# Optimization experiments

Hardware: AMD Instinct MI355X
Metric: run time of the kernel (lower is better)

Reference implementation:

```python
import jax, jax.numpy as jnp
import numpy as np

B, T, HE, H = 32, 2048, 512, 512


def setup_inputs() -> dict:
    key = jax.random.key(0)
    ks = jax.random.split(key, 10)
    s_e = 1.0 / np.sqrt(HE)
    s_h = 1.0 / np.sqrt(H)
    return {
        "x": jax.random.normal(ks[0], (B, T, HE), dtype=jnp.float32),
        "wu_i": jax.random.normal(ks[1], (HE, H), dtype=jnp.float32) * s_e,
        "wu_h": jax.random.normal(ks[2], (H, H), dtype=jnp.float32) * s_h,
        "bu": jax.random.normal(ks[3], (H,), dtype=jnp.float32) * s_h,
        "wr_i": jax.random.normal(ks[4], (HE, H), dtype=jnp.float32) * s_e,
        "wr_h": jax.random.normal(ks[5], (H, H), dtype=jnp.float32) * s_h,
        "br": jax.random.normal(ks[6], (H,), dtype=jnp.float32) * s_h,
        "wc_i": jax.random.normal(ks[7], (HE, H), dtype=jnp.float32) * s_e,
        "wc_h": jax.random.normal(ks[8], (H, H), dtype=jnp.float32) * s_h,
        "bc": jax.random.normal(ks[9], (H,), dtype=jnp.float32) * s_h,
    }


def reference(x, wu_i, wu_h, bu, wr_i, wr_h, br, wc_i, wc_h, bc):
    # Precompute input projections for all timesteps (one big GEMM each).
    u_in_x = jnp.einsum("bte,eh->bth", x, wu_i) + bu  # (B,T,H)
    r_in_x = jnp.einsum("bte,eh->bth", x, wr_i) + br
    c_in_x = jnp.einsum("bte,eh->bth", x, wc_i) + bc

    h0 = jnp.zeros((x.shape[0], wu_h.shape[0]), dtype=x.dtype)

    def step(h_prev, inputs):
        u_x, r_x, c_x = inputs
        u = jax.nn.sigmoid(u_x + h_prev @ wu_h)
        r = jax.nn.sigmoid(r_x + h_prev @ wr_h)
        # Faithful to source: r * (h_prev @ wc_h) (reset applied after matmul)
        c = jnp.tanh(c_x + r * (h_prev @ wc_h))
        h = (1.0 - u) * h_prev + u * c
        return h, h

    # scan over time: move T to leading axis
    xs = (
        jnp.swapaxes(u_in_x, 0, 1),
        jnp.swapaxes(r_in_x, 0, 1),
        jnp.swapaxes(c_in_x, 0, 1),
    )
    _, ys = jax.lax.scan(step, h0, xs)  # ys: (T,B,H)
    return jnp.swapaxes(ys, 0, 1)  # (B,T,H)
```

## Files before the change

### kernel.cpp

```cpp
#include <hip/hip_runtime.h>
#include <hip/hip_bf16.h>
#include <hip/hip_fp16.h>
#include <stdint.h>

#define BB 32
#define TT 2048
#define HH 512
#define MM (BB*TT)

typedef __attribute__((ext_vector_type(8))) short bf16x8;
typedef __attribute__((ext_vector_type(4))) float f32x4;
typedef __attribute__((ext_vector_type(2))) float f32x2;
typedef __attribute__((ext_vector_type(4))) unsigned short us4;
typedef __attribute__((ext_vector_type(8))) unsigned short us8;
typedef unsigned long long u64;

__device__ __forceinline__ unsigned short f2bf(float f) {
  __hip_bfloat16 h = __float2bfloat16(f);
  return *reinterpret_cast<unsigned short*>(&h);
}
__device__ __forceinline__ float bf2f(unsigned short u) {
  return __uint_as_float(((unsigned int)u) << 16);
}

__device__ __forceinline__ void wg_barrier_lgkm() {
  asm volatile("s_waitcnt lgkmcnt(0)\n\ts_barrier" ::: "memory");
}

__device__ __forceinline__ float fast_sigmoid(float x) {
  float e = __expf(-x);
  return __builtin_amdgcn_rcpf(1.f + e);
}
__device__ __forceinline__ float fast_tanh(float x) {
  float xc = fminf(fmaxf(x, -15.f), 15.f);
  float e2 = __expf(2.f * xc);
  return (e2 - 1.f) * __builtin_amdgcn_rcpf(e2 + 1.f);
}

__global__ void wconv_kernel(const float* __restrict__ wu, const float* __restrict__ wr,
                             const float* __restrict__ wc,
                             unsigned short* __restrict__ wuT, unsigned short* __restrict__ wrT,
                             unsigned short* __restrict__ wcTh, unsigned short* __restrict__ wcTl) {
  int idx = blockIdx.x * 256 + threadIdx.x;
  int n = idx >> 9, k = idx & 511;
  int src = k * HH + n;
  wuT[idx] = f2bf(wu[src]);
  wrT[idx] = f2bf(wr[src]);
  float v = wc[src];
  unsigned short hi = f2bf(v);
  wcTh[idx] = hi;
  wcTl[idx] = f2bf(v - bf2f(hi));
}

template<int MODE>
__global__ __launch_bounds__(256) void proj_gemm(
    const float* __restrict__ X,
    const unsigned short* __restrict__ B0T,
    const unsigned short* __restrict__ B1T,
    const float* __restrict__ bias0,
    const float* __restrict__ bias1,
    void* __restrict__ outp) {
  __shared__ __attribute__((aligned(16))) unsigned short Ah[128][72];
  __shared__ __attribute__((aligned(16))) unsigned short Al[128][72];
  __shared__ __attribute__((aligned(16))) unsigned short Bs0[64][72];
  __shared__ __attribute__((aligned(16))) unsigned short Bs1[64][72];
  const int tid = threadIdx.x;
  const int w = tid >> 6, l = tid & 63;
  const int lr = l & 15, lk = l >> 4;
  const int rowBase = blockIdx.x * 128;
  const int colBase = blockIdx.y * 64;

  f32x4 acc0[2][4], acc1[2][4];
  const f32x4 zero = {0.f, 0.f, 0.f, 0.f};
  #pragma unroll
  for (int m = 0; m < 2; ++m)
    #pragma unroll
    for (int n = 0; n < 4; ++n) { acc0[m][n] = zero; acc1[m][n] = zero; }

  for (int kt = 0; kt < 8; ++kt) {
    #pragma unroll
    for (int i = 0; i < 8; ++i) {
      int idx = tid + 256 * i;
      int r = idx >> 4, c4 = idx & 15;
      float4 v = *reinterpret_cast<const float4*>(
          X + (size_t)(rowBase + r) * HH + kt * 64 + c4 * 4);
      us4 hv;
      hv.x = f2bf(v.x); hv.y = f2bf(v.y); hv.z = f2bf(v.z); hv.w = f2bf(v.w);
      *reinterpret_cast<us4*>(&Ah[r][c4 * 4]) = hv;
      if (MODE == 1) {
        us4 lv;
        lv.x = f2bf(v.x - bf2f(hv.x)); lv.y = f2bf(v.y - bf2f(hv.y));
        lv.z = f2bf(v.z - bf2f(hv.z)); lv.w = f2bf(v.w - bf2f(hv.w));
        *reinterpret_cast<us4*>(&Al[r][c4 * 4]) = lv;
      }
    }
    #pragma unroll
    for (int i = 0; i < 2; ++i) {
      int idx = tid + 256 * i;
      int n = idx >> 3, k8 = idx & 7;
      const size_t go = (size_t)(colBase + n) * HH + kt * 64 + k8 * 8;
      *reinterpret_cast<us8*>(&Bs0[n][k8 * 8]) = *reinterpret_cast<const us8*>(B0T + go);
      *reinterpret_cast<us8*>(&Bs1[n][k8 * 8]) = *reinterpret_cast<const us8*>(B1T + go);
    }
    __syncthreads();
    #pragma unroll
    for (int ks = 0; ks < 2; ++ks) {
      const int k0 = ks * 32 + lk * 8;
      bf16x8 a[2], b0[4], b1[4];
      #pragma unroll
      for (int m = 0; m < 2; ++m)
        a[m] = *reinterpret_cast<const bf16x8*>(&Ah[32 * w + 16 * m + lr][k0]);
      #pragma unroll
      for (int n = 0; n < 4; ++n) {
        b0[n] = *reinterpret_cast<const bf16x8*>(&Bs0[16 * n + lr][k0]);
        b1[n] = *reinterpret_cast<const bf16x8*>(&Bs1[16 * n + lr][k0]);
      }
      if (MODE == 1) {
        bf16x8 al[2];
        #pragma unroll
        for (int m = 0; m < 2; ++m)
          al[m] = *reinterpret_cast<const bf16x8*>(&Al[32 * w + 16 * m + lr][k0]);
        #pragma unroll
        for (int m = 0; m < 2; ++m)
          #pragma unroll
          for (int n = 0; n < 4; ++n) {
            acc0[m][n] = __builtin_amdgcn_mfma_f32_16x16x32_bf16(a[m],  b0[n], acc0[m][n], 0, 0, 0);
            acc0[m][n] = __builtin_amdgcn_mfma_f32_16x16x32_bf16(a[m],  b1[n], acc0[m][n], 0, 0, 0);
            acc0[m][n] = __builtin_amdgcn_mfma_f32_16x16x32_bf16(al[m], b0[n], acc0[m][n], 0, 0, 0);
          }
      } else {
        #pragma unroll
        for (int m = 0; m < 2; ++m)
          #pragma unroll
          for (int n = 0; n < 4; ++n) {
            acc0[m][n] = __builtin_amdgcn_mfma_f32_16x16x32_bf16(a[m], b0[n], acc0[m][n], 0, 0, 0);
            acc1[m][n] = __builtin_amdgcn_mfma_f32_16x16x32_bf16(a[m], b1[n], acc1[m][n], 0, 0, 0);
          }
      }
    }
    __syncthreads();
  }
  #pragma unroll
  for (int m = 0; m < 2; ++m) {
    #pragma unroll
    for (int n = 0; n < 4; ++n) {
      const int col = colBase + 16 * n + lr;
      const float bv0 = bias0[col];
      const float bv1 = (MODE == 0) ? bias1[col] : 0.f;
      #pragma unroll
      for (int q = 0; q < 4; ++q) {
        const int row = rowBase + 32 * w + 16 * m + lk * 4 + q;
        const size_t o = (size_t)row * HH + col;
        if (MODE == 0) {
          float v0 = acc0[m][n][q] + bv0;
          float v1 = acc1[m][n][q] + bv1;
          unsigned int pk = (unsigned int)__half_as_ushort(__float2half(v0)) |
                            ((unsigned int)__half_as_ushort(__float2half(v1)) << 16);
          reinterpret_cast<unsigned int*>(outp)[o] = pk;
        } else {
          reinterpret_cast<__half*>(outp)[o] = __float2half(acc0[m][n][q] + bv0);
        }
      }
    }
  }
}

__global__ __launch_bounds__(512, 2) void scan_kernel(
    const float* __restrict__ wu_h, const float* __restrict__ wr_h,
    const float* __restrict__ wc_h,
    float* __restrict__ out, const __half* __restrict__ cx,
    u64* __restrict__ hslow) {
  const int blk = blockIdx.x;
  const int b = (blk & 7) + ((blk >> 6) << 3);
  const int g = (blk >> 3) & 7;
  const int tid = threadIdx.x;
  const int w = tid >> 6, l = tid & 63;
  const int jg = g * 64 + l;
  const int jp = w * 64 + l;
  const size_t bo = (size_t)b * TT * HH;

  f32x2 wu2[32], wr2[32], wc2[32];
  #pragma unroll
  for (int i = 0; i < 32; ++i) {
    const size_t o0 = (size_t)(w * 64 + 2 * i) * HH + jg;
    wu2[i] = f32x2{wu_h[o0], wu_h[o0 + HH]};
    wr2[i] = f32x2{wr_h[o0], wr_h[o0 + HH]};
    wc2[i] = f32x2{wc_h[o0], wc_h[o0 + HH]};
  }

  __shared__ float parts[2][8][3][64];
  __shared__ unsigned int  stag_urx[64];
  __shared__ unsigned short stag_cx[64];

  unsigned int* outu = reinterpret_cast<unsigned int*>(out);
  const unsigned short* cxu = reinterpret_cast<const unsigned short*>(cx);

  unsigned int urx_p = 0;
  unsigned short cx_p = 0;
  if (w == 1) {
    urx_p = outu[bo + jg];
    cx_p  = cxu[bo + jg];
  }

  float hprev = 0.f;
  u64* const poll = hslow + (size_t)b * HH + jp;
  u64* const pub  = hslow + (size_t)b * HH + jg;
  const bool out_duty = (g == 1);

  for (int t = 0; t < TT; ++t) {
    float hval = 0.f;
    if (t > 0) {
      u64 v;
      for (;;) {
        v = __hip_atomic_load(poll + (size_t)(t & 1) * (BB * HH),
                              __ATOMIC_RELAXED, __HIP_MEMORY_SCOPE_AGENT);
        if (__all((int)((unsigned int)(v >> 32) >= (unsigned int)t))) break;
      }
      hval = __uint_as_float((unsigned int)v);
      if (out_duty)
        out[bo + (size_t)(t - 1) * HH + jp] = hval;
    }
    if (w == 1) {
      stag_urx[l] = urx_p;
      stag_cx[l]  = cx_p;
      if (t + 1 < TT) {
        urx_p = outu[bo + (size_t)(t + 1) * HH + jg];
        cx_p  = cxu[bo + (size_t)(t + 1) * HH + jg];
      }
    }
    f32x2 au2 = {0.f, 0.f}, ar2 = {0.f, 0.f}, ac2 = {0.f, 0.f};
    const unsigned int hbits = __float_as_uint(hval);
    #pragma unroll
    for (int i = 0; i < 32; ++i) {
      f32x2 hp;
      hp.x = __uint_as_float(__builtin_amdgcn_readlane(hbits, 2 * i));
      hp.y = __uint_as_float(__builtin_amdgcn_readlane(hbits, 2 * i + 1));
      au2 = __builtin_elementwise_fma(hp, wu2[i], au2);
      ar2 = __builtin_elementwise_fma(hp, wr2[i], ar2);
      ac2 = __builtin_elementwise_fma(hp, wc2[i], ac2);
    }
    const int pb = t & 1;
    parts[pb][w][0][l] = au2.x + au2.y;
    parts[pb][w][1][l] = ar2.x + ar2.y;
    parts[pb][w][2][l] = ac2.x + ac2.y;
    wg_barrier_lgkm();
    if (w == 0) {
      float su = 0.f, sr = 0.f, sc = 0.f;
      #pragma unroll
      for (int ww = 0; ww < 8; ++ww) {
        su += parts[pb][ww][0][l];
        sr += parts[pb][ww][1][l];
        sc += parts[pb][ww][2][l];
      }
      const unsigned int urx_c = stag_urx[l];
      const unsigned short cx_c = stag_cx[l];
      const float ux = __half2float(__ushort_as_half((unsigned short)(urx_c & 0xffffu)));
      const float rx = __half2float(__ushort_as_half((unsigned short)(urx_c >> 16)));
      const float cxf = __half2float(__ushort_as_half(cx_c));
      const float uu = fast_sigmoid(su + ux);
      const float rr = fast_sigmoid(sr + rx);
      const float ccv = fast_tanh(cxf + rr * sc);
      const float h = hprev + uu * (ccv - hprev);
      hprev = h;
      const u64 pv = ((u64)(unsigned int)(t + 1) << 32) | (u64)__float_as_uint(h);
      __hip_atomic_store(pub + (size_t)((t + 1) & 1) * (BB * HH), pv,
                         __ATOMIC_RELAXED, __HIP_MEMORY_SCOPE_AGENT);
    }
  }
  if (w == 0)
    out[bo + (size_t)(TT - 1) * HH + jg] = hprev;
}

extern "C" void kernel_launch(void* const* d_in, const int* in_sizes, int n_in,
                              void* d_out, int out_size, void* d_ws, size_t ws_size,
                              hipStream_t stream) {
  const float* x    = (const float*)d_in[0];
  const float* wu_i = (const float*)d_in[1];
  const float* wu_h = (const float*)d_in[2];
  const float* bu   = (const float*)d_in[3];
  const float* wr_i = (const float*)d_in[4];
  const float* wr_h = (const float*)d_in[5];
  const float* br   = (const float*)d_in[6];
  const float* wc_i = (const float*)d_in[7];
  const float* wc_h = (const float*)d_in[8];
  const float* bc   = (const float*)d_in[9];
  float* out = (float*)d_out;

  char* ws = (char*)d_ws;
  __half* cx = (__half*)ws;
  unsigned short* wuT  = (unsigned short*)(ws + (size_t)MM * HH * 2);
  unsigned short* wrT  = wuT + HH * HH;
  unsigned short* wcTh = wrT + HH * HH;
  unsigned short* wcTl = wcTh + HH * HH;
  u64* hslow = (u64*)(wcTl + HH * HH);

  hipMemsetAsync(hslow, 0, (size_t)2 * BB * HH * sizeof(u64), stream);
  wconv_kernel<<<1024, 256, 0, stream>>>(wu_i, wr_i, wc_i, wuT, wrT, wcTh, wcTl);
  proj_gemm<0><<<dim3(MM / 128, 8), 256, 0, stream>>>(x, wuT, wrT, bu, br, (void*)out);
  proj_gemm<1><<<dim3(MM / 128, 8), 256, 0, stream>>>(x, wcTh, wcTl, bc, bc, (void*)cx);

  void* args[] = { (void*)&wu_h, (void*)&wr_h, (void*)&wc_h, (void*)&out,
                   (void*)&cx, (void*)&hslow };
  hipLaunchCooperativeKernel((void*)scan_kernel, dim3(256), dim3(512), args, 0, stream);
}
```

Baseline: 3.714 ms.

## Distribute gate reduction across all waves and double-buffer staging

The cross-wave reduction and gate computation, previously done serially by wave 0 over 8 partial sums, is now spread across all 8 waves. Each wave owns 8 columns, and eight row-groups of 8 lanes each take one wave's partial and combine them with xor shuffles. The staging buffers become double-buffered by timestep parity, which makes the single-barrier schedule safe. The spin-poll keeps two loads in flight to cut the latency of seeing a new state. The goal is to shorten the serial critical path per timestep, at the cost of extra shuffles and padded shared memory.

```diff
diff --git a/kernel.cpp b/kernel.cpp
--- a/kernel.cpp
+++ b/kernel.cpp
@@ -35,6 +35,10 @@
   float xc = fminf(fmaxf(x, -15.f), 15.f);
   float e2 = __expf(2.f * xc);
   return (e2 - 1.f) * __builtin_amdgcn_rcpf(e2 + 1.f);
+}
+
+__device__ __forceinline__ u64 agent_ld(const u64* p) {
+  return __hip_atomic_load(p, __ATOMIC_RELAXED, __HIP_MEMORY_SCOPE_AGENT);
 }
 
 __global__ void wconv_kernel(const float* __restrict__ wu, const float* __restrict__ wr,
@@ -177,6 +181,9 @@
   const int w = tid >> 6, l = tid & 63;
   const int jg = g * 64 + l;
   const int jp = w * 64 + l;
+  const int cl = l & 7;
+  const int colw = 8 * w + cl;
+  const int pprime = l >> 3;
   const size_t bo = (size_t)b * TT * HH;
 
   f32x2 wu2[32], wr2[32], wc2[32];
@@ -188,9 +195,9 @@
     wc2[i] = f32x2{wc_h[o0], wc_h[o0 + HH]};
   }
 
-  __shared__ float parts[2][8][3][64];
-  __shared__ unsigned int  stag_urx[64];
-  __shared__ unsigned short stag_cx[64];
+  __shared__ float parts[2][8][3][72];
+  __shared__ unsigned int  stag_urx[2][64];
+  __shared__ unsigned short stag_cx[2][64];
 
   unsigned int* outu = reinterpret_cast<unsigned int*>(out);
   const unsigned short* cxu = reinterpret_cast<const unsigned short*>(cx);
@@ -204,25 +211,30 @@
 
   float hprev = 0.f;
   u64* const poll = hslow + (size_t)b * HH + jp;
-  u64* const pub  = hslow + (size_t)b * HH + jg;
+  u64* const pub  = hslow + (size_t)b * HH + 64 * g + colw;
   const bool out_duty = (g == 1);
 
   for (int t = 0; t < TT; ++t) {
+    const int pb = t & 1;
     float hval = 0.f;
     if (t > 0) {
+      const u64* pp = poll + (size_t)pb * (BB * HH);
+      u64 va = agent_ld(pp);
+      u64 vb = agent_ld(pp);
       u64 v;
       for (;;) {
-        v = __hip_atomic_load(poll + (size_t)(t & 1) * (BB * HH),
-                              __ATOMIC_RELAXED, __HIP_MEMORY_SCOPE_AGENT);
-        if (__all((int)((unsigned int)(v >> 32) >= (unsigned int)t))) break;
+        if (__all((int)((unsigned int)(va >> 32) >= (unsigned int)t))) { v = va; break; }
+        va = agent_ld(pp);
+        if (__all((int)((unsigned int)(vb >> 32) >= (unsigned int)t))) { v = vb; break; }
+        vb = agent_ld(pp);
       }
       hval = __uint_as_float((unsigned int)v);
       if (out_duty)
         out[bo + (size_t)(t - 1) * HH + jp] = hval;
     }
     if (w == 1) {
-      stag_urx[l] = urx_p;
-      stag_cx[l]  = cx_p;
+      stag_urx[pb][l] = urx_p;
+      stag_cx[pb][l]  = cx_p;
       if (t + 1 < TT) {
         urx_p = outu[bo + (size_t)(t + 1) * HH + jg];
         cx_p  = cxu[bo + (size_t)(t + 1) * HH + jg];
@@ -239,36 +251,36 @@
       ar2 = __builtin_elementwise_fma(hp, wr2[i], ar2);
       ac2 = __builtin_elementwise_fma(hp, wc2[i], ac2);
     }
-    const int pb = t & 1;
     parts[pb][w][0][l] = au2.x + au2.y;
     parts[pb][w][1][l] = ar2.x + ar2.y;
     parts[pb][w][2][l] = ac2.x + ac2.y;
     wg_barrier_lgkm();
-    if (w == 0) {
-      float su = 0.f, sr = 0.f, sc = 0.f;
-      #pragma unroll
-      for (int ww = 0; ww < 8; ++ww) {
-        su += parts[pb][ww][0][l];
-        sr += parts[pb][ww][1][l];
-        sc += parts[pb][ww][2][l];
-      }
-      const unsigned int urx_c = stag_urx[l];
-      const unsigned short cx_c = stag_cx[l];
-      const float ux = __half2float(__ushort_as_half((unsigned short)(urx_c & 0xffffu)));
-      const float rx = __half2float(__ushort_as_half((unsigned short)(urx_c >> 16)));
-      const float cxf = __half2float(__ushort_as_half(cx_c));
-      const float uu = fast_sigmoid(su + ux);
-      const float rr = fast_sigmoid(sr + rx);
-      const float ccv = fast_tanh(cxf + rr * sc);
-      const float h = hprev + uu * (ccv - hprev);
-      hprev = h;
-      const u64 pv = ((u64)(unsigned int)(t + 1) << 32) | (u64)__float_as_uint(h);
+    float su = parts[pb][pprime][0][colw];
+    float sr = parts[pb][pprime][1][colw];
+    float sc = parts[pb][pprime][2][colw];
+    #pragma unroll
+    for (int m = 8; m <= 32; m <<= 1) {
+      su += __shfl_xor(su, m, 64);
+      sr += __shfl_xor(sr, m, 64);
+      sc += __shfl_xor(sc, m, 64);
+    }
+    const unsigned int urx_c = stag_urx[pb][colw];
+    const unsigned short cx_c = stag_cx[pb][colw];
+    const float ux = __half2float(__ushort_as_half((unsigned short)(urx_c & 0xffffu)));
+    const float rx = __half2float(__ushort_as_half((unsigned short)(urx_c >> 16)));
+    const float cxf = __half2float(__ushort_as_half(cx_c));
+    const float uu = fast_sigmoid(su + ux);
+    const float rr = fast_sigmoid(sr + rx);
+    const float ccv = fast_tanh(cxf + rr * sc);
+    const float h = hprev + uu * (ccv - hprev);
+    hprev = h;
+    const u64 pv = ((u64)(unsigned int)(t + 1) << 32) | (u64)__float_as_uint(h);
+    if (l < 8)
       __hip_atomic_store(pub + (size_t)((t + 1) & 1) * (BB * HH), pv,
                          __ATOMIC_RELAXED, __HIP_MEMORY_SCOPE_AGENT);
-    }
-  }
-  if (w == 0)
-    out[bo + (size_t)(TT - 1) * HH + jg] = hprev;
+  }
+  if (l < 8)
+    out[bo + (size_t)(TT - 1) * HH + 64 * g + colw] = hprev;
 }
 
 extern "C" void kernel_launch(void* const* d_in, const int* in_sizes, int n_in,
```

After: 6.730 ms. 81.2% more time.
